# Optimization experiments

Measured on AMD Instinct MI355X. Metric: run time of the kernel, lower is better.

## Reference

```python
import jax, jax.numpy as jnp
import numpy as np

B, LQ, LV = 32, 64, 128
QS, FS, BN = 512, 1024, 512

def setup_inputs() -> dict:
    key = jax.random.key(0)
    k1, k2, k3, k4, k5 = jax.random.split(key, 5)
    s = lambda n: 1.0 / np.sqrt(n)
    return {
        "phr_feats": jax.random.normal(k1, (B, LQ, QS), dtype=jnp.float32),
        "vis_feats": jax.random.normal(k2, (B, LV, FS), dtype=jnp.float32),
        "W": jax.random.uniform(k3, (BN, QS), jnp.float32, -s(QS), s(QS)),
        "U": jax.random.uniform(k4, (BN, FS), jnp.float32, -s(FS), s(FS)),
        "b": jnp.ones((BN,), dtype=jnp.float32),
        "w": jax.random.uniform(k5, (1, BN), jnp.float32, -s(BN), s(BN)),
    }

def reference(phr_feats, vis_feats, W, U, b, w):
    # Wh: [B,Lq,BN], Uv: [B,Lv,BN]
    Wh = jnp.einsum('bqd,nd->bqn', phr_feats, W)
    Uv = jnp.einsum('bvf,nf->bvn', vis_feats, U)
    # broadcast add + tanh: [B,Lq,Lv,BN]
    t = jnp.tanh(Wh[:, :, None, :] + Uv[:, None, :, :] + b)
    energies = jnp.einsum('bqvn,n->bqv', t, w[0])  # squeeze(-1)
    weights = jax.nn.softmax(energies, axis=2)
    aligned = jnp.einsum('bqv,bvf->bqf', weights, vis_feats)
    semantic_group_feats = jnp.concatenate([phr_feats, aligned], axis=2)
    return (semantic_group_feats, weights, energies)
```

## Files before the change

kernel.cpp:

```cpp
#include <hip/hip_runtime.h>

#define NB  32
#define NLQ 64
#define NLV 128
#define NQS 512
#define NFS 1024
#define NBN 512
#define CC  2.8853900817779268f

typedef float  floatx4 __attribute__((ext_vector_type(4)));
typedef __bf16 bf16x8  __attribute__((ext_vector_type(8)));
typedef unsigned short us;

__device__ __forceinline__ us f2bf(float f) {
    unsigned int u = __float_as_uint(f);
    u += 0x7fffu + ((u >> 16) & 1u);
    return (us)(u >> 16);
}
__device__ __forceinline__ unsigned int pktrunc(float lo, float hi) {
    return __builtin_amdgcn_perm(__float_as_uint(hi), __float_as_uint(lo), 0x07060302u);
}
__device__ __forceinline__ float blo(unsigned int u) {
    return __uint_as_float(u << 16);
}
__device__ __forceinline__ float bhi(unsigned int u) {
    return __uint_as_float(u & 0xffff0000u);
}

__device__ __forceinline__ void gemm64(
    us* smem,
    const float* __restrict__ A, const float* __restrict__ Bt,
    const float* __restrict__ bias,
    float* __restrict__ whYp, us* __restrict__ uvYTp,
    int K, int bx, int by, float* __restrict__ sgf)
{
    us* As = smem;
    us* Bs = smem + 64 * 40;
    const int tid  = threadIdx.x;
    const int m0   = bx * 64;
    const int n0   = by * 64;
    const int wave = tid >> 6;
    const int lane = tid & 63;
    const int wm   = (wave >> 1) * 32;
    const int wn   = (wave & 1) * 32;
    const int srow = tid >> 2;
    const int sk   = (tid & 3) * 8;
    const int fm   = lane & 15;
    const int fko  = (lane >> 4) * 8;

    floatx4 acc[2][2] = {};
    const float* ag = A  + (size_t)(m0 + srow) * K + sk;
    const float* bg = Bt + (size_t)(n0 + srow) * K + sk;

    float4 a0 = *(const float4*)(ag),     a1 = *(const float4*)(ag + 4);
    float4 b0 = *(const float4*)(bg),     b1 = *(const float4*)(bg + 4);

    for (int k0 = 0; k0 < K; k0 += 32) {
        __syncthreads();
        if (sgf) {
            float* d = sgf + (size_t)(m0 + srow) * (NQS + NFS) + k0 + sk;
            *(float4*)d       = a0;
            *(float4*)(d + 4) = a1;
        }
        uint4 av = { pktrunc(a0.x, a0.y), pktrunc(a0.z, a0.w),
                     pktrunc(a1.x, a1.y), pktrunc(a1.z, a1.w) };
        uint4 bv = { pktrunc(b0.x, b0.y), pktrunc(b0.z, b0.w),
                     pktrunc(b1.x, b1.y), pktrunc(b1.z, b1.w) };
        *(uint4*)(As + srow * 40 + sk) = av;
        *(uint4*)(Bs + srow * 40 + sk) = bv;
        const int kn = k0 + 32;
        if (kn < K) {
            a0 = *(const float4*)(ag + kn); a1 = *(const float4*)(ag + kn + 4);
            b0 = *(const float4*)(bg + kn); b1 = *(const float4*)(bg + kn + 4);
        }
        __syncthreads();
        bf16x8 am[2], bn[2];
        #pragma unroll
        for (int i = 0; i < 2; ++i)
            am[i] = *(const bf16x8*)(As + (wm + 16 * i + fm) * 40 + fko);
        #pragma unroll
        for (int j = 0; j < 2; ++j)
            bn[j] = *(const bf16x8*)(Bs + (wn + 16 * j + fm) * 40 + fko);
        #pragma unroll
        for (int i = 0; i < 2; ++i)
            #pragma unroll
            for (int j = 0; j < 2; ++j)
                acc[i][j] = __builtin_amdgcn_mfma_f32_16x16x32_bf16(am[i], bn[j], acc[i][j], 0, 0, 0);
    }

    const int cr = (lane >> 4) * 4;
    const int cc = lane & 15;
    if (whYp) {
        #pragma unroll
        for (int j = 0; j < 2; ++j) {
            int gn = n0 + wn + 16 * j + cc;
            float bj = bias[gn];
            #pragma unroll
            for (int i = 0; i < 2; ++i)
                #pragma unroll
                for (int r = 0; r < 4; ++r) {
                    int gm = m0 + wm + 16 * i + cr + r;
                    whYp[(size_t)gm * NBN + gn] =
                        __builtin_amdgcn_exp2f(CC * (acc[i][j][r] + bj));
                }
        }
    } else {
        us* Cs = smem;
        __syncthreads();
        #pragma unroll
        for (int i = 0; i < 2; ++i)
            #pragma unroll
            for (int j = 0; j < 2; ++j) {
                int nl = wn + 16 * j + cc;
                int vl = wm + 16 * i + cr;
                #pragma unroll
                for (int r = 0; r < 4; ++r)
                    Cs[nl * 72 + vl + r] =
                        f2bf(__builtin_amdgcn_exp2f(CC * acc[i][j][r]));
            }
        __syncthreads();
        const int bb    = m0 >> 7;
        const int vbase = m0 & 127;
        const int nl    = tid >> 2;
        const int vc    = (tid & 3) * 16;
        uint4 t0 = *(const uint4*)(Cs + nl * 72 + vc);
        uint4 t1 = *(const uint4*)(Cs + nl * 72 + vc + 8);
        us* dst = uvYTp + ((size_t)bb * NBN + n0 + nl) * NLV + vbase + vc;
        *(uint4*)dst       = t0;
        *(uint4*)(dst + 8) = t1;
    }
}

__global__ __launch_bounds__(256) void gemm_both(
    const float* __restrict__ phr, const float* __restrict__ W,
    const float* __restrict__ bias,
    const float* __restrict__ vis, const float* __restrict__ U,
    float* __restrict__ whY, us* __restrict__ uvYT,
    float* __restrict__ out_sgf)
{
    __shared__ __align__(16) us smem[2 * 64 * 40];
    int blk = blockIdx.x;
    if (blk < 256) {
        int bx = blk % 32, by = blk / 32;
        gemm64(smem, phr, W, bias, whY, nullptr, NQS, bx, by,
               by == 0 ? out_sgf : nullptr);
    } else {
        blk -= 256;
        int bx = blk % 64, by = blk / 64;
        gemm64(smem, vis, U, bias, nullptr, uvYT, NFS, bx, by, nullptr);
    }
}

__global__ __launch_bounds__(512) void energize(
    const float* __restrict__ whY,
    const us* __restrict__ uvYT,
    const float* __restrict__ wvec,
    float* __restrict__ out_w, float* __restrict__ out_e,
    us* __restrict__ p_bf, us* __restrict__ p_lo)
{
    const float LOG2E = 1.4426950408889634f;
    int blk = blockIdx.x;
    blk = (blk & 7) * 64 + (blk >> 3);
    const int b    = blk >> 4;
    const int qq4  = blk & 15;
    const int tid  = threadIdx.x;
    const int wave = __builtin_amdgcn_readfirstlane(tid >> 6);
    const int lane = tid & 63;
    const int q0   = qq4 * 4;

    __shared__ float part[4][8][NLV];

    float4 sw0 = *(const float4*)(wvec + lane * 8);
    float4 sw1 = *(const float4*)(wvec + lane * 8 + 4);
    float sumw = sw0.x + sw0.y + sw0.z + sw0.w + sw1.x + sw1.y + sw1.z + sw1.w;
    #pragma unroll
    for (int off = 32; off; off >>= 1) sumw += __shfl_xor(sumw, off);

    const float* yqp = whY + (size_t)(b * NLQ + q0) * NBN + wave * 64;
    const float* wp  = wvec + wave * 64;
    const us*    uvp = uvYT + ((size_t)b * NBN + wave * 64) * NLV + 2 * lane;

    float acc[4][2] = {};
    #pragma unroll 2
    for (int nc = 0; nc < 64; nc += 8) {
        unsigned int yv[8];
        #pragma unroll
        for (int k = 0; k < 8; ++k)
            yv[k] = *(const unsigned int*)(uvp + (size_t)(nc + k) * NLV);
        #pragma unroll
        for (int kk = 0; kk < 4; ++kk) {
            const int k0 = nc + 2 * kk, k1 = k0 + 1;
            float x0a = blo(yv[2 * kk]),     x0b = bhi(yv[2 * kk]);
            float x1a = blo(yv[2 * kk + 1]), x1b = bhi(yv[2 * kk + 1]);
            float w0 = wp[k0], w1 = wp[k1];
            #pragma unroll
            for (int q = 0; q < 4; ++q) {
                float y0 = yqp[q * NBN + k0];
                float y1 = yqp[q * NBN + k1];
                float d0a = fmaf(x0a, y0, 1.f), d1a = fmaf(x1a, y1, 1.f);
                float d0b = fmaf(x0b, y0, 1.f), d1b = fmaf(x1b, y1, 1.f);
                float numa = fmaf(w0, d1a, w1 * d0a);
                float numb = fmaf(w0, d1b, w1 * d0b);
                acc[q][0] = fmaf(numa, __builtin_amdgcn_rcpf(d0a * d1a), acc[q][0]);
                acc[q][1] = fmaf(numb, __builtin_amdgcn_rcpf(d0b * d1b), acc[q][1]);
            }
        }
    }
    #pragma unroll
    for (int q = 0; q < 4; ++q) {
        float2 t = { acc[q][0], acc[q][1] };
        *(float2*)&part[q][wave][2 * lane] = t;
    }
    __syncthreads();

    if (wave < 4) {
        const int q = wave;
        float s0 = 0.f, s1 = 0.f;
        #pragma unroll
        for (int nq = 0; nq < 8; ++nq) {
            s0 += part[q][nq][2 * lane];
            s1 += part[q][nq][2 * lane + 1];
        }
        float e0 = sumw - 2.f * s0;
        float e1 = sumw - 2.f * s1;
        float m = fmaxf(e0, e1);
        #pragma unroll
        for (int off = 32; off; off >>= 1) m = fmaxf(m, __shfl_xor(m, off));
        float x0 = __builtin_amdgcn_exp2f((e0 - m) * LOG2E);
        float x1 = __builtin_amdgcn_exp2f((e1 - m) * LOG2E);
        float ss = x0 + x1;
        #pragma unroll
        for (int off = 32; off; off >>= 1) ss += __shfl_xor(ss, off);
        float inv = __builtin_amdgcn_rcpf(ss);
        float p0 = x0 * inv, p1 = x1 * inv;

        const size_t row = (size_t)(b * NLQ + q0 + q);
        float2 ep = { e0, e1 };
        float2 pp = { p0, p1 };
        *(float2*)(out_e + row * NLV + 2 * lane) = ep;
        *(float2*)(out_w + row * NLV + 2 * lane) = pp;
        unsigned int pb0 = f2bf(p0), pb1 = f2bf(p1);
        float lo0 = p0 - __uint_as_float(pb0 << 16);
        float lo1 = p1 - __uint_as_float(pb1 << 16);
        unsigned int lb0 = f2bf(lo0), lb1 = f2bf(lo1);
        *(unsigned int*)(p_bf + row * NLV + 2 * lane) = pb0 | (pb1 << 16);
        *(unsigned int*)(p_lo + row * NLV + 2 * lane) = lb0 | (lb1 << 16);
    }
}

__global__ __launch_bounds__(256) void aligned_mfma(
    const us* __restrict__ p_bf, const us* __restrict__ p_lo,
    const float* __restrict__ vis,
    float* __restrict__ out_sgf)
{
    int blk = blockIdx.x;
    blk = (blk & 7) * 64 + (blk >> 3);
    const int b    = blk >> 4;
    const int ft   = blk & 15;
    const int tid  = threadIdx.x;
    const int wave = tid >> 6;
    const int lane = tid & 63;
    const int wm   = (wave >> 1) * 32;
    const int wf   = (wave & 1) * 32;
    const int fm   = lane & 15;
    const int fko  = (lane >> 4) * 8;

    __shared__ us Vs[64][136];

    {
        const int v  = tid >> 1;
        const int fh = (tid & 1) * 32;
        const float* vp = vis + ((size_t)b * NLV + v) * NFS + ft * 64 + fh;
        #pragma unroll
        for (int r = 0; r < 8; ++r) {
            float4 x = ((const float4*)vp)[r];
            Vs[fh + 4 * r + 0][v] = (us)(__float_as_uint(x.x) >> 16);
            Vs[fh + 4 * r + 1][v] = (us)(__float_as_uint(x.y) >> 16);
            Vs[fh + 4 * r + 2][v] = (us)(__float_as_uint(x.z) >> 16);
            Vs[fh + 4 * r + 3][v] = (us)(__float_as_uint(x.w) >> 16);
        }
    }
    __syncthreads();

    floatx4 acc[2][2] = {};
    const us* pA  = p_bf + ((size_t)b * NLQ + wm + fm) * NLV + fko;
    const us* pAl = p_lo + ((size_t)b * NLQ + wm + fm) * NLV + fko;

    #pragma unroll
    for (int ks = 0; ks < 4; ++ks) {
        bf16x8 a[2], al[2], bb2[2];
        #pragma unroll
        for (int i = 0; i < 2; ++i) {
            a[i]  = *(const bf16x8*)(pA  + (size_t)i * 16 * NLV + ks * 32);
            al[i] = *(const bf16x8*)(pAl + (size_t)i * 16 * NLV + ks * 32);
        }
        #pragma unroll
        for (int j = 0; j < 2; ++j)
            bb2[j] = *(const bf16x8*)&Vs[wf + 16 * j + fm][ks * 32 + fko];
        #pragma unroll
        for (int i = 0; i < 2; ++i)
            #pragma unroll
            for (int j = 0; j < 2; ++j) {
                acc[i][j] = __builtin_amdgcn_mfma_f32_16x16x32_bf16(a[i],  bb2[j], acc[i][j], 0, 0, 0);
                acc[i][j] = __builtin_amdgcn_mfma_f32_16x16x32_bf16(al[i], bb2[j], acc[i][j], 0, 0, 0);
            }
    }

    const int cr = (lane >> 4) * 4;
    const int cc = lane & 15;
    #pragma unroll
    for (int i = 0; i < 2; ++i)
        #pragma unroll
        for (int j = 0; j < 2; ++j)
            #pragma unroll
            for (int r = 0; r < 4; ++r) {
                int q = wm + 16 * i + cr + r;
                int f = ft * 64 + wf + 16 * j + cc;
                size_t row = (size_t)b * NLQ + q;
                out_sgf[row * (NQS + NFS) + NQS + f] = acc[i][j][r];
            }
}

extern "C" void kernel_launch(void* const* d_in, const int* in_sizes, int n_in,
                              void* d_out, int out_size, void* d_ws, size_t ws_size,
                              hipStream_t stream) {
    const float* phr  = (const float*)d_in[0];
    const float* vis  = (const float*)d_in[1];
    const float* W    = (const float*)d_in[2];
    const float* U    = (const float*)d_in[3];
    const float* bias = (const float*)d_in[4];
    const float* wvec = (const float*)d_in[5];

    char* ws = (char*)d_ws;
    float* whY  = (float*)ws;
    us* uvYT    = (us*)(ws + (4u << 20));
    us* p_bf    = (us*)(ws + (8u << 20));
    us* p_lo    = (us*)(ws + (8u << 20) + (512u << 10));

    float* out     = (float*)d_out;
    float* out_sgf = out;
    float* out_w   = out_sgf + (size_t)NB * NLQ * (NQS + NFS);
    float* out_e   = out_w   + (size_t)NB * NLQ * NLV;

    gemm_both<<<768, 256, 0, stream>>>(phr, W, bias, vis, U, whY, uvYT, out_sgf);
    energize<<<512, 512, 0, stream>>>(whY, uvYT, wvec, out_w, out_e, p_bf, p_lo);
    aligned_mfma<<<512, 256, 0, stream>>>(p_bf, p_lo, vis, out_sgf);
}
```

Before: 124.9 us.

## Pre-convert inputs to bf16 and stage GEMM tiles via direct global-to-LDS loads

Adds a separate pass that converts phr, vis, W and U to bf16 in workspace and also writes the phr part of the concatenated output. The GEMM then streams bf16 tiles straight into LDS using global_load_lds with an XOR-style swizzle, replacing register prefetch and in-loop packing. The aligned kernel reads the bf16 copy of vis. The goal is to halve GEMM input traffic and remove conversion work from the main loop. In exchange it adds an extra launch and a full read/write pass over the inputs, and drops the register double-buffering.

```diff
diff --git a/kernel.cpp b/kernel.cpp
--- a/kernel.cpp
+++ b/kernel.cpp
@@ -11,6 +11,8 @@
 typedef float  floatx4 __attribute__((ext_vector_type(4)));
 typedef __bf16 bf16x8  __attribute__((ext_vector_type(8)));
 typedef unsigned short us;
+typedef __attribute__((address_space(1))) const unsigned int gu32;
+typedef __attribute__((address_space(3))) unsigned int lu32;
 
 __device__ __forceinline__ us f2bf(float f) {
     unsigned int u = __float_as_uint(f);
@@ -27,15 +29,44 @@
     return __uint_as_float(u & 0xffff0000u);
 }
 
+#define PHR4 262144
+#define VIS4 1048576
+#define WW4  65536
+#define UU4  131072
+#define TOT4 (PHR4 + VIS4 + WW4 + UU4)
+
+__global__ __launch_bounds__(256) void convert_bf16(
+    const float* __restrict__ phr, const float* __restrict__ vis,
+    const float* __restrict__ W,   const float* __restrict__ U,
+    us* __restrict__ phr_b, us* __restrict__ vis_b,
+    us* __restrict__ W_b,   us* __restrict__ U_b,
+    float* __restrict__ out_sgf)
+{
+    int i = blockIdx.x * 256 + threadIdx.x;
+    if (i >= TOT4) return;
+    const float* src; us* dst; int o;
+    if (i < PHR4)              { src = phr; dst = phr_b; o = i; }
+    else if (i < PHR4 + VIS4)  { src = vis; dst = vis_b; o = i - PHR4; }
+    else if (i < PHR4 + VIS4 + WW4) { src = W; dst = W_b; o = i - PHR4 - VIS4; }
+    else                       { src = U; dst = U_b; o = i - PHR4 - VIS4 - WW4; }
+    float4 v = ((const float4*)src)[o];
+    uint2 r = { pktrunc(v.x, v.y), pktrunc(v.z, v.w) };
+    *(uint2*)(dst + (size_t)o * 4) = r;
+    if (i < PHR4) {
+        int row = o >> 7, c4 = o & 127;
+        ((float4*)out_sgf)[(size_t)row * 384 + c4] = v;
+    }
+}
+
 __device__ __forceinline__ void gemm64(
     us* smem,
-    const float* __restrict__ A, const float* __restrict__ Bt,
+    const us* __restrict__ A, const us* __restrict__ Bt,
     const float* __restrict__ bias,
     float* __restrict__ whYp, us* __restrict__ uvYTp,
-    int K, int bx, int by, float* __restrict__ sgf)
+    int K, int bx, int by)
 {
     us* As = smem;
-    us* Bs = smem + 64 * 40;
+    us* Bs = smem + 2048;
     const int tid  = threadIdx.x;
     const int m0   = bx * 64;
     const int n0   = by * 64;
@@ -43,44 +74,35 @@
     const int lane = tid & 63;
     const int wm   = (wave >> 1) * 32;
     const int wn   = (wave & 1) * 32;
-    const int srow = tid >> 2;
-    const int sk   = (tid & 3) * 8;
     const int fm   = lane & 15;
-    const int fko  = (lane >> 4) * 8;
+    const int c16  = lane >> 4;
+
+    const int srow   = tid >> 2;
+    const int scol16 = ((tid & 3) - srow - (srow >> 2)) & 3;
+    const us* ga = A  + (size_t)(m0 + srow) * K + scol16 * 8;
+    const us* gb = Bt + (size_t)(n0 + srow) * K + scol16 * 8;
 
     floatx4 acc[2][2] = {};
-    const float* ag = A  + (size_t)(m0 + srow) * K + sk;
-    const float* bg = Bt + (size_t)(n0 + srow) * K + sk;
-
-    float4 a0 = *(const float4*)(ag),     a1 = *(const float4*)(ag + 4);
-    float4 b0 = *(const float4*)(bg),     b1 = *(const float4*)(bg + 4);
-
     for (int k0 = 0; k0 < K; k0 += 32) {
         __syncthreads();
-        if (sgf) {
-            float* d = sgf + (size_t)(m0 + srow) * (NQS + NFS) + k0 + sk;
-            *(float4*)d       = a0;
-            *(float4*)(d + 4) = a1;
-        }
-        uint4 av = { pktrunc(a0.x, a0.y), pktrunc(a0.z, a0.w),
-                     pktrunc(a1.x, a1.y), pktrunc(a1.z, a1.w) };
-        uint4 bv = { pktrunc(b0.x, b0.y), pktrunc(b0.z, b0.w),
-                     pktrunc(b1.x, b1.y), pktrunc(b1.z, b1.w) };
-        *(uint4*)(As + srow * 40 + sk) = av;
-        *(uint4*)(Bs + srow * 40 + sk) = bv;
-        const int kn = k0 + 32;
-        if (kn < K) {
-            a0 = *(const float4*)(ag + kn); a1 = *(const float4*)(ag + kn + 4);
-            b0 = *(const float4*)(bg + kn); b1 = *(const float4*)(bg + kn + 4);
-        }
+        __builtin_amdgcn_global_load_lds((gu32*)(ga + k0),
+                                         (lu32*)(As + wave * 512), 16, 0, 0);
+        __builtin_amdgcn_global_load_lds((gu32*)(gb + k0),
+                                         (lu32*)(Bs + wave * 512), 16, 0, 0);
         __syncthreads();
         bf16x8 am[2], bn[2];
         #pragma unroll
-        for (int i = 0; i < 2; ++i)
-            am[i] = *(const bf16x8*)(As + (wm + 16 * i + fm) * 40 + fko);
-        #pragma unroll
-        for (int j = 0; j < 2; ++j)
-            bn[j] = *(const bf16x8*)(Bs + (wn + 16 * j + fm) * 40 + fko);
+        for (int i = 0; i < 2; ++i) {
+            int r  = wm + 16 * i + fm;
+            int sl = (c16 + r + (r >> 2)) & 3;
+            am[i] = *(const bf16x8*)(As + r * 32 + sl * 8);
+        }
+        #pragma unroll
+        for (int j = 0; j < 2; ++j) {
+            int r  = wn + 16 * j + fm;
+            int sl = (c16 + r + (r >> 2)) & 3;
+            bn[j] = *(const bf16x8*)(Bs + r * 32 + sl * 8);
+        }
         #pragma unroll
         for (int i = 0; i < 2; ++i)
             #pragma unroll
@@ -132,22 +154,20 @@
 }
 
 __global__ __launch_bounds__(256) void gemm_both(
-    const float* __restrict__ phr, const float* __restrict__ W,
+    const us* __restrict__ phr_b, const us* __restrict__ W_b,
     const float* __restrict__ bias,
-    const float* __restrict__ vis, const float* __restrict__ U,
-    float* __restrict__ whY, us* __restrict__ uvYT,
-    float* __restrict__ out_sgf)
-{
-    __shared__ __align__(16) us smem[2 * 64 * 40];
+    const us* __restrict__ vis_b, const us* __restrict__ U_b,
+    float* __restrict__ whY, us* __restrict__ uvYT)
+{
+    __shared__ __align__(16) us smem[4608];
     int blk = blockIdx.x;
     if (blk < 256) {
         int bx = blk % 32, by = blk / 32;
-        gemm64(smem, phr, W, bias, whY, nullptr, NQS, bx, by,
-               by == 0 ? out_sgf : nullptr);
+        gemm64(smem, phr_b, W_b, bias, whY, nullptr, NQS, bx, by);
     } else {
         blk -= 256;
         int bx = blk % 64, by = blk / 64;
-        gemm64(smem, vis, U, bias, nullptr, uvYT, NFS, bx, by, nullptr);
+        gemm64(smem, vis_b, U_b, bias, nullptr, uvYT, NFS, bx, by);
     }
 }
 
@@ -250,7 +270,7 @@
 
 __global__ __launch_bounds__(256) void aligned_mfma(
     const us* __restrict__ p_bf, const us* __restrict__ p_lo,
-    const float* __restrict__ vis,
+    const us* __restrict__ vis_b,
     float* __restrict__ out_sgf)
 {
     int blk = blockIdx.x;
@@ -270,14 +290,14 @@
     {
         const int v  = tid >> 1;
         const int fh = (tid & 1) * 32;
-        const float* vp = vis + ((size_t)b * NLV + v) * NFS + ft * 64 + fh;
+        const us* vp = vis_b + ((size_t)b * NLV + v) * NFS + ft * 64 + fh;
         #pragma unroll
         for (int r = 0; r < 8; ++r) {
-            float4 x = ((const float4*)vp)[r];
-            Vs[fh + 4 * r + 0][v] = (us)(__float_as_uint(x.x) >> 16);
-            Vs[fh + 4 * r + 1][v] = (us)(__float_as_uint(x.y) >> 16);
-            Vs[fh + 4 * r + 2][v] = (us)(__float_as_uint(x.z) >> 16);
-            Vs[fh + 4 * r + 3][v] = (us)(__float_as_uint(x.w) >> 16);
+            uint2 u = *(const uint2*)(vp + 4 * r);
+            Vs[fh + 4 * r + 0][v] = (us)(u.x & 0xffffu);
+            Vs[fh + 4 * r + 1][v] = (us)(u.x >> 16);
+            Vs[fh + 4 * r + 2][v] = (us)(u.y & 0xffffu);
+            Vs[fh + 4 * r + 3][v] = (us)(u.y >> 16);
         }
     }
     __syncthreads();
@@ -332,17 +352,23 @@
     const float* wvec = (const float*)d_in[5];
 
     char* ws = (char*)d_ws;
-    float* whY  = (float*)ws;
-    us* uvYT    = (us*)(ws + (4u << 20));
-    us* p_bf    = (us*)(ws + (8u << 20));
-    us* p_lo    = (us*)(ws + (8u << 20) + (512u << 10));
+    us* phr_b   = (us*)ws;
+    us* vis_b   = (us*)(ws + (2u << 20));
+    us* W_b     = (us*)(ws + (10u << 20));
+    us* U_b     = (us*)(ws + (10u << 20) + (512u << 10));
+    float* whY  = (float*)(ws + (12u << 20));
+    us* uvYT    = (us*)(ws + (16u << 20));
+    us* p_bf    = (us*)(ws + (20u << 20));
+    us* p_lo    = (us*)(ws + (20u << 20) + (512u << 10));
 
     float* out     = (float*)d_out;
     float* out_sgf = out;
     float* out_w   = out_sgf + (size_t)NB * NLQ * (NQS + NFS);
     float* out_e   = out_w   + (size_t)NB * NLQ * NLV;
 
-    gemm_both<<<768, 256, 0, stream>>>(phr, W, bias, vis, U, whY, uvYT, out_sgf);
+    convert_bf16<<<TOT4 / 256, 256, 0, stream>>>(
+        phr, vis, W, U, phr_b, vis_b, W_b, U_b, out_sgf);
+    gemm_both<<<768, 256, 0, stream>>>(phr_b, W_b, bias, vis_b, U_b, whY, uvYT);
     energize<<<512, 512, 0, stream>>>(whY, uvYT, wvec, out_w, out_e, p_bf, p_lo);
-    aligned_mfma<<<512, 256, 0, stream>>>(p_bf, p_lo, vis, out_sgf);
-}
+    aligned_mfma<<<512, 256, 0, stream>>>(p_bf, p_lo, vis_b, out_sgf);
+}
```

Result: no change. 125.4 us (+0.3%).

## Triple-buffer GEMM tiles with 64-wide K steps and XOR-swizzled LDS

Applied to the files above, without the earlier changes.

Reworks the projection GEMM main loop to use K tiles of 64 instead of 32, three LDS buffers so conversion and store of the next tile overlap MFMA on the current one, and an XOR swizzle on LDS columns in place of row padding. Each iteration needs one barrier instead of two, and global loads are issued two tiles ahead. This is meant to hide global-load latency and cut barrier overhead in the GEMM phase. It raises LDS use to 48KB per block and adds register pressure, which may reduce occupancy. The epilogue's reuse of smem (Cs) is in lines not shown.

```diff
diff --git a/kernel.cpp b/kernel.cpp
--- a/kernel.cpp
+++ b/kernel.cpp
@@ -34,8 +34,6 @@
     float* __restrict__ whYp, us* __restrict__ uvYTp,
     int K, int bx, int by, float* __restrict__ sgf)
 {
-    us* As = smem;
-    us* Bs = smem + 64 * 40;
     const int tid  = threadIdx.x;
     const int m0   = bx * 64;
     const int n0   = by * 64;
@@ -43,50 +41,98 @@
     const int lane = tid & 63;
     const int wm   = (wave >> 1) * 32;
     const int wn   = (wave & 1) * 32;
-    const int srow = tid >> 2;
-    const int sk   = (tid & 3) * 8;
     const int fm   = lane & 15;
-    const int fko  = (lane >> 4) * 8;
-
+    const int c16  = lane >> 4;
+
+    const int row = tid >> 2;
+    const int kq  = tid & 3;
+    const int c0p = ((kq * 2)     ^ (row & 7)) * 8;
+    const int c1p = ((kq * 2 + 1) ^ (row & 7)) * 8;
+    const int rb64 = row * 64;
+    const float* gA = A  + (size_t)(m0 + row) * K + kq * 16;
+    const float* gB = Bt + (size_t)(n0 + row) * K + kq * 16;
+
+    float4 ra[4], rb[4];
     floatx4 acc[2][2] = {};
-    const float* ag = A  + (size_t)(m0 + srow) * K + sk;
-    const float* bg = Bt + (size_t)(n0 + srow) * K + sk;
-
-    float4 a0 = *(const float4*)(ag),     a1 = *(const float4*)(ag + 4);
-    float4 b0 = *(const float4*)(bg),     b1 = *(const float4*)(bg + 4);
-
-    for (int k0 = 0; k0 < K; k0 += 32) {
-        __syncthreads();
-        if (sgf) {
-            float* d = sgf + (size_t)(m0 + srow) * (NQS + NFS) + k0 + sk;
-            *(float4*)d       = a0;
-            *(float4*)(d + 4) = a1;
-        }
-        uint4 av = { pktrunc(a0.x, a0.y), pktrunc(a0.z, a0.w),
-                     pktrunc(a1.x, a1.y), pktrunc(a1.z, a1.w) };
-        uint4 bv = { pktrunc(b0.x, b0.y), pktrunc(b0.z, b0.w),
-                     pktrunc(b1.x, b1.y), pktrunc(b1.z, b1.w) };
-        *(uint4*)(As + srow * 40 + sk) = av;
-        *(uint4*)(Bs + srow * 40 + sk) = bv;
-        const int kn = k0 + 32;
-        if (kn < K) {
-            a0 = *(const float4*)(ag + kn); a1 = *(const float4*)(ag + kn + 4);
-            b0 = *(const float4*)(bg + kn); b1 = *(const float4*)(bg + kn + 4);
-        }
-        __syncthreads();
-        bf16x8 am[2], bn[2];
-        #pragma unroll
-        for (int i = 0; i < 2; ++i)
-            am[i] = *(const bf16x8*)(As + (wm + 16 * i + fm) * 40 + fko);
-        #pragma unroll
-        for (int j = 0; j < 2; ++j)
-            bn[j] = *(const bf16x8*)(Bs + (wn + 16 * j + fm) * 40 + fko);
-        #pragma unroll
-        for (int i = 0; i < 2; ++i)
-            #pragma unroll
-            for (int j = 0; j < 2; ++j)
-                acc[i][j] = __builtin_amdgcn_mfma_f32_16x16x32_bf16(am[i], bn[j], acc[i][j], 0, 0, 0);
-    }
+    const int nt = K >> 6;
+
+#define LOADT(k0) do {                                                         \
+    ra[0] = *(const float4*)(gA + (k0));      ra[1] = *(const float4*)(gA + (k0) + 4);  \
+    ra[2] = *(const float4*)(gA + (k0) + 8);  ra[3] = *(const float4*)(gA + (k0) + 12); \
+    rb[0] = *(const float4*)(gB + (k0));      rb[1] = *(const float4*)(gB + (k0) + 4);  \
+    rb[2] = *(const float4*)(gB + (k0) + 8);  rb[3] = *(const float4*)(gB + (k0) + 12); \
+} while (0)
+
+#define CVTWR(bufbase) do {                                                    \
+    us* as_ = (bufbase);  us* bs_ = (bufbase) + 4096;                          \
+    uint4 ca0 = { pktrunc(ra[0].x, ra[0].y), pktrunc(ra[0].z, ra[0].w),        \
+                  pktrunc(ra[1].x, ra[1].y), pktrunc(ra[1].z, ra[1].w) };      \
+    uint4 ca1 = { pktrunc(ra[2].x, ra[2].y), pktrunc(ra[2].z, ra[2].w),        \
+                  pktrunc(ra[3].x, ra[3].y), pktrunc(ra[3].z, ra[3].w) };      \
+    uint4 cb0 = { pktrunc(rb[0].x, rb[0].y), pktrunc(rb[0].z, rb[0].w),        \
+                  pktrunc(rb[1].x, rb[1].y), pktrunc(rb[1].z, rb[1].w) };      \
+    uint4 cb1 = { pktrunc(rb[2].x, rb[2].y), pktrunc(rb[2].z, rb[2].w),        \
+                  pktrunc(rb[3].x, rb[3].y), pktrunc(rb[3].z, rb[3].w) };      \
+    *(uint4*)(as_ + rb64 + c0p) = ca0;  *(uint4*)(as_ + rb64 + c1p) = ca1;     \
+    *(uint4*)(bs_ + rb64 + c0p) = cb0;  *(uint4*)(bs_ + rb64 + c1p) = cb1;     \
+} while (0)
+
+#define SGFWR(k0) do {                                                         \
+    if (sgf) {                                                                 \
+        float* d = sgf + (size_t)(m0 + row) * (NQS + NFS) + (k0) + kq * 16;    \
+        *(float4*)d        = ra[0];  *(float4*)(d + 4)  = ra[1];               \
+        *(float4*)(d + 8)  = ra[2];  *(float4*)(d + 12) = ra[3];               \
+    }                                                                          \
+} while (0)
+
+    LOADT(0);
+    CVTWR(smem);
+    SGFWR(0);
+    if (nt > 1) LOADT(64);
+    asm volatile("s_waitcnt lgkmcnt(0)" ::: "memory");
+    __builtin_amdgcn_s_barrier();
+    __builtin_amdgcn_sched_barrier(0);
+
+    int rs = 0;
+    for (int t = 0; t < nt; ++t) {
+        us* As = smem + rs * 8192;
+        us* Bs = As + 4096;
+        if (t + 1 < nt) {
+            int ws = rs + 1; if (ws >= 3) ws -= 3;
+            CVTWR(smem + ws * 8192);
+            SGFWR((t + 1) * 64);
+            if (t + 2 < nt) LOADT((t + 2) * 64);
+        }
+        __builtin_amdgcn_sched_barrier(0);
+        #pragma unroll
+        for (int ks = 0; ks < 2; ++ks) {
+            bf16x8 am[2], bn[2];
+            #pragma unroll
+            for (int i = 0; i < 2; ++i) {
+                int r  = wm + 16 * i + fm;
+                int pc = (ks * 4 + c16) ^ (r & 7);
+                am[i] = *(const bf16x8*)(As + r * 64 + pc * 8);
+            }
+            #pragma unroll
+            for (int j = 0; j < 2; ++j) {
+                int r  = wn + 16 * j + fm;
+                int pc = (ks * 4 + c16) ^ (r & 7);
+                bn[j] = *(const bf16x8*)(Bs + r * 64 + pc * 8);
+            }
+            #pragma unroll
+            for (int i = 0; i < 2; ++i)
+                #pragma unroll
+                for (int j = 0; j < 2; ++j)
+                    acc[i][j] = __builtin_amdgcn_mfma_f32_16x16x32_bf16(am[i], bn[j], acc[i][j], 0, 0, 0);
+        }
+        asm volatile("s_waitcnt lgkmcnt(0)" ::: "memory");
+        __builtin_amdgcn_s_barrier();
+        __builtin_amdgcn_sched_barrier(0);
+        rs = (rs == 2) ? 0 : rs + 1;
+    }
+#undef LOADT
+#undef CVTWR
+#undef SGFWR
 
     const int cr = (lane >> 4) * 4;
     const int cc = lane & 15;
@@ -138,7 +184,7 @@
     float* __restrict__ whY, us* __restrict__ uvYT,
     float* __restrict__ out_sgf)
 {
-    __shared__ __align__(16) us smem[2 * 64 * 40];
+    __shared__ __align__(16) us smem[24576];
     int blk = blockIdx.x;
     if (blk < 256) {
         int bx = blk % 32, by = blk / 32;
```

After: 131.8 us. 5.4% more time.
